# Performance work log

Measured on AMD Instinct MI355X. Metric: run time of the kernel, lower is better.

Reference implementation:

```python
import jax, jax.numpy as jnp
import numpy as np

B, N_NODE, FN, FE = 8, 128, 64, 64  # batch, n_node, n_node_fea, n_edge_fea


def setup_inputs() -> dict:
    key = jax.random.key(0)
    k = jax.random.split(key, 7)
    stdv_w = 1.0 / np.sqrt(2 * FN + FE)  # torch reset uses 1/sqrt(size(0))
    stdv_b = 1.0 / np.sqrt(FN)
    return {
        "H": jax.random.normal(k[0], (B, N_NODE, FN), jnp.float32),
        "A": jax.random.uniform(k[1], (B, N_NODE, N_NODE), jnp.float32),
        "E": jax.random.normal(k[2], (B, N_NODE, N_NODE, FE), jnp.float32),
        "W_att": jax.random.uniform(k[3], (2 * FN + FE, FN), jnp.float32, -stdv_w, stdv_w),
        "W_nei": jax.random.uniform(k[4], (2 * FN + FE, FN), jnp.float32, -stdv_w, stdv_w),
        "bias_att": jax.random.uniform(k[5], (FN,), jnp.float32, -stdv_b, stdv_b),
        "bias_nei": jax.random.uniform(k[6], (FN,), jnp.float32, -stdv_b, stdv_b),
        "N": N_NODE,
    }


def _branch(H, A, E, W, bias, fn):
    # (A[...,None] * cat(H_i, H_j, E)) @ W + bias, computed without
    # materializing the [B,N,N,2F+Fe] concat: split W into row blocks.
    f = H.shape[-1]
    Wi, Wj, We = W[:f], W[f:2 * f], W[2 * f:]
    proj = (
        jnp.einsum('bif,fl->bil', H, Wi)[:, :, None, :]   # H_i broadcast over j
        + jnp.einsum('bjf,fl->bjl', H, Wj)[:, None, :, :] # H_j broadcast over i
        + jnp.einsum('bije,el->bijl', E, We)
    )
    return A[..., None] * proj + bias  # [B, N, N, F]


def reference(H, A, E, W_att, W_nei, bias_att, bias_nei, N):
    att = _branch(H, A, E, W_att, bias_att, None)
    conv = _branch(H, A, E, W_nei, bias_nei, None)
    gated = jax.nn.sigmoid(att) * jax.nn.relu(conv)  # [B, N, N, F]
    return jnp.sum(gated, axis=1)  # sum over first node axis -> [B, N, F]
```

## Files before the change

### kernel.cpp

```cpp
#include <hip/hip_runtime.h>


typedef _Float16 half8 __attribute__((ext_vector_type(8)));
typedef float floatx4 __attribute__((ext_vector_type(4)));

__device__ __forceinline__ half8 cvt2(const float4 a, const float4 b) {
  half8 v;
  v[0] = (_Float16)a.x; v[1] = (_Float16)a.y; v[2] = (_Float16)a.z; v[3] = (_Float16)a.w;
  v[4] = (_Float16)b.x; v[5] = (_Float16)b.y; v[6] = (_Float16)b.z; v[7] = (_Float16)b.w;
  return v;
}

__global__ __launch_bounds__(256, 2)
void amp_fused(const float* __restrict__ H, const float* __restrict__ A,
               const float* __restrict__ E,
               const float* __restrict__ Wa, const float* __restrict__ Wn,
               const float* __restrict__ ba, const float* __restrict__ bn,
               float* __restrict__ out) {
  const int bx = blockIdx.x;
  const int b = bx >> 6;
  const int rem = bx & 63;
  const int jt = rem >> 3;
  const int ch = rem & 7;
  const int w = threadIdx.x >> 6;
  const int lane = threadIdx.x & 63;
  const int quad = lane >> 4;
  const int l15 = lane & 15;
  const int i0b = ch * 16;
  const int i0 = i0b + w * 4;
  const int j0 = jt * 16;
  const float* Wptr[2] = {Wa, Wn};

  __shared__ __align__(16) char smem[48 * 1024];
  _Float16* fraglds = reinterpret_cast<_Float16*>(smem);
  float* pflds = reinterpret_cast<float*>(smem);
  float* pjlds = reinterpret_cast<float*>(smem + 8 * 1024);
  float (*red)[16][64] = reinterpret_cast<float (*)[16][64]>(smem);

  half8 hi[2], hj[2];
  {
    const float* hib = H + (b * 128 + i0b + l15) * 64 + quad * 8;
    const float* hjb = H + (b * 128 + j0 + l15) * 64 + quad * 8;
#pragma unroll
    for (int hh = 0; hh < 2; ++hh) {
      hi[hh] = cvt2(*reinterpret_cast<const float4*>(hib + hh * 32),
                    *reinterpret_cast<const float4*>(hib + hh * 32 + 4));
      hj[hh] = cvt2(*reinterpret_cast<const float4*>(hjb + hh * 32),
                    *reinterpret_cast<const float4*>(hjb + hh * 32 + 4));
    }
  }

#pragma unroll
  for (int k = 0; k < 12; ++k) {
    const int F = w * 12 + k;
    const int kind = F >> 4;
    const int f = F & 15;
    const int br = f >> 3;
    const int t = (f >> 1) & 3;
    const int hh = f & 1;
    const float* src = Wptr[br] + (kind * 64 + hh * 32 + quad * 8) * 64 + t * 16 + l15;
    half8 v;
#pragma unroll
    for (int x = 0; x < 8; ++x) v[x] = (_Float16)src[x * 64];
    *reinterpret_cast<half8*>(fraglds + F * 512 + lane * 8) = v;
  }
  __syncthreads();

  floatx4 pif[2], pjf[2];
#pragma unroll
  for (int pp = 0; pp < 2; ++pp) {
    const int p = w * 2 + pp;
    const int br = p >> 2;
    const int t = p & 3;
    floatx4 z = {0.f, 0.f, 0.f, 0.f};
    pif[pp] = z; pjf[pp] = z;
#pragma unroll
    for (int hh = 0; hh < 2; ++hh) {
      half8 bi = *reinterpret_cast<half8*>(fraglds + (br * 8 + t * 2 + hh) * 512 + lane * 8);
      half8 bj = *reinterpret_cast<half8*>(fraglds + (16 + br * 8 + t * 2 + hh) * 512 + lane * 8);
      pif[pp] = __builtin_amdgcn_mfma_f32_16x16x32_f16(hi[hh], bi, pif[pp], 0, 0, 0);
      pjf[pp] = __builtin_amdgcn_mfma_f32_16x16x32_f16(hj[hh], bj, pjf[pp], 0, 0, 0);
    }
  }
  __syncthreads();
#pragma unroll
  for (int pp = 0; pp < 2; ++pp) {
    const int p = w * 2 + pp;
    *reinterpret_cast<floatx4*>(pflds + (p * 64 + lane) * 4) = pif[pp];
    *reinterpret_cast<floatx4*>(pjlds + (p * 64 + lane) * 4) = pjf[pp];
  }
  __syncthreads();

  float pia_all[2][4][4];
  float pj[2][4][4];
  half8 wf[2][4][2];
#pragma unroll
  for (int br = 0; br < 2; ++br)
#pragma unroll
    for (int t = 0; t < 4; ++t) {
      const int p = br * 4 + t;
      const floatx4 pjv = *reinterpret_cast<const floatx4*>(pjlds + (p * 64 + lane) * 4);
      const floatx4 piv = *reinterpret_cast<const floatx4*>(pflds + (p * 64 + w * 16 + l15) * 4);
#pragma unroll
      for (int r = 0; r < 4; ++r) { pj[br][t][r] = pjv[r]; pia_all[br][t][r] = piv[r]; }
#pragma unroll
      for (int hh = 0; hh < 2; ++hh)
        wf[br][t][hh] = *reinterpret_cast<half8*>(
            fraglds + (32 + br * 8 + t * 2 + hh) * 512 + lane * 8);
    }

  float biasv[2][4];
#pragma unroll
  for (int t = 0; t < 4; ++t) {
    biasv[0][t] = ba[t * 16 + l15];
    biasv[1][t] = bn[t * 16 + l15];
  }

  float acc[4][4];
#pragma unroll
  for (int t = 0; t < 4; ++t)
#pragma unroll
    for (int r = 0; r < 4; ++r) acc[t][r] = 0.f;

#pragma unroll
  for (int ii = 0; ii < 4; ++ii) {
    const int i = i0 + ii;
    const float* erow = E + ((size_t)((b * 128 + i) * 128 + j0 + l15)) * 64 + quad * 8;
    half8 a0 = cvt2(*reinterpret_cast<const float4*>(erow),
                    *reinterpret_cast<const float4*>(erow + 4));
    half8 a1 = cvt2(*reinterpret_cast<const float4*>(erow + 32),
                    *reinterpret_cast<const float4*>(erow + 36));

    const float4 av4 = *reinterpret_cast<const float4*>(
        A + (b * 128 + i) * 128 + j0 + quad * 4);
    const float av[4] = {av4.x, av4.y, av4.z, av4.w};

#pragma unroll
    for (int t = 0; t < 4; ++t) {
      floatx4 z = {0.f, 0.f, 0.f, 0.f};
      floatx4 pa = __builtin_amdgcn_mfma_f32_16x16x32_f16(a0, wf[0][t][0], z, 0, 0, 0);
      pa = __builtin_amdgcn_mfma_f32_16x16x32_f16(a1, wf[0][t][1], pa, 0, 0, 0);
      floatx4 pn = __builtin_amdgcn_mfma_f32_16x16x32_f16(a0, wf[1][t][0], z, 0, 0, 0);
      pn = __builtin_amdgcn_mfma_f32_16x16x32_f16(a1, wf[1][t][1], pn, 0, 0, 0);
#pragma unroll
      for (int r = 0; r < 4; ++r) {
        float att = av[r] * (pa[r] + pia_all[0][t][ii] + pj[0][t][r]) + biasv[0][t];
        float cnv = av[r] * (pn[r] + pia_all[1][t][ii] + pj[1][t][r]) + biasv[1][t];
        float ex = __expf(-att);
        float sig = __builtin_amdgcn_rcpf(1.0f + ex);
        acc[t][r] += sig * fmaxf(cnv, 0.f);
      }
    }
  }

  __syncthreads();
#pragma unroll
  for (int t = 0; t < 4; ++t)
#pragma unroll
    for (int r = 0; r < 4; ++r)
      red[w][quad * 4 + r][t * 16 + l15] = acc[t][r];
  __syncthreads();

  const int tid = threadIdx.x;
#pragma unroll
  for (int k = 0; k < 4; ++k) {
    int idx = k * 256 + tid;
    int jl = idx >> 6;
    int l = idx & 63;
    float s = red[0][jl][l] + red[1][jl][l] + red[2][jl][l] + red[3][jl][l];
    atomicAdd(out + (b * 128 + j0 + jl) * 64 + l, s);
  }
}

extern "C" void kernel_launch(void* const* d_in, const int* in_sizes, int n_in,
                              void* d_out, int out_size, void* d_ws, size_t ws_size,
                              hipStream_t stream) {
  const float* H = (const float*)d_in[0];
  const float* A = (const float*)d_in[1];
  const float* E = (const float*)d_in[2];
  const float* Wa = (const float*)d_in[3];
  const float* Wn = (const float*)d_in[4];
  const float* ba = (const float*)d_in[5];
  const float* bn = (const float*)d_in[6];
  float* out = (float*)d_out;

  hipMemsetAsync(d_out, 0, (size_t)out_size * sizeof(float), stream);
  amp_fused<<<512, 256, 0, stream>>>(H, A, E, Wa, Wn, ba, bn, out);
}
```

Measured before the change: 97.46 us.

## Prefetch first E/A rows before weight staging and trim conversions and barriers

Loads the E and A data for the first two i-rows, plus the bias values, at kernel start, so their global-memory latency overlaps the weight fp16 staging and the H projections. The projection scratch moves to its own LDS region (64KB total), which removes one barrier; another barrier before the reduction writes is also dropped. Float-to-half conversions now use packed round-toward-zero instructions, which slightly changes rounding. The prefetched data raises register pressure under the 2-blocks-per-CU launch bound.

```diff
diff --git a/kernel.cpp b/kernel.cpp
--- a/kernel.cpp
+++ b/kernel.cpp
@@ -2,13 +2,16 @@
 
 
 typedef _Float16 half8 __attribute__((ext_vector_type(8)));
+typedef __fp16 fp16x2 __attribute__((ext_vector_type(2)));
 typedef float floatx4 __attribute__((ext_vector_type(4)));
 
 __device__ __forceinline__ half8 cvt2(const float4 a, const float4 b) {
-  half8 v;
-  v[0] = (_Float16)a.x; v[1] = (_Float16)a.y; v[2] = (_Float16)a.z; v[3] = (_Float16)a.w;
-  v[4] = (_Float16)b.x; v[5] = (_Float16)b.y; v[6] = (_Float16)b.z; v[7] = (_Float16)b.w;
-  return v;
+  union { fp16x2 h2[4]; half8 h8; } u;
+  u.h2[0] = __builtin_amdgcn_cvt_pkrtz(a.x, a.y);
+  u.h2[1] = __builtin_amdgcn_cvt_pkrtz(a.z, a.w);
+  u.h2[2] = __builtin_amdgcn_cvt_pkrtz(b.x, b.y);
+  u.h2[3] = __builtin_amdgcn_cvt_pkrtz(b.z, b.w);
+  return u.h8;
 }
 
 __global__ __launch_bounds__(256, 2)
@@ -31,11 +34,30 @@
   const int j0 = jt * 16;
   const float* Wptr[2] = {Wa, Wn};
 
-  __shared__ __align__(16) char smem[48 * 1024];
+  __shared__ __align__(16) char smem[64 * 1024];
   _Float16* fraglds = reinterpret_cast<_Float16*>(smem);
-  float* pflds = reinterpret_cast<float*>(smem);
-  float* pjlds = reinterpret_cast<float*>(smem + 8 * 1024);
+  float* pflds = reinterpret_cast<float*>(smem + 48 * 1024);
+  float* pjlds = reinterpret_cast<float*>(smem + 56 * 1024);
   float (*red)[16][64] = reinterpret_cast<float (*)[16][64]>(smem);
+
+  float4 e_pf[2][4];
+  float4 a_pf[2];
+#pragma unroll
+  for (int ii = 0; ii < 2; ++ii) {
+    const float* erow = E + ((size_t)((b * 128 + i0 + ii) * 128 + j0 + l15)) * 64 + quad * 8;
+    e_pf[ii][0] = *reinterpret_cast<const float4*>(erow);
+    e_pf[ii][1] = *reinterpret_cast<const float4*>(erow + 4);
+    e_pf[ii][2] = *reinterpret_cast<const float4*>(erow + 32);
+    e_pf[ii][3] = *reinterpret_cast<const float4*>(erow + 36);
+    a_pf[ii] = *reinterpret_cast<const float4*>(A + (b * 128 + i0 + ii) * 128 + j0 + quad * 4);
+  }
+
+  float biasv[2][4];
+#pragma unroll
+  for (int t = 0; t < 4; ++t) {
+    biasv[0][t] = ba[t * 16 + l15];
+    biasv[1][t] = bn[t * 16 + l15];
+  }
 
   half8 hi[2], hj[2];
   {
@@ -59,10 +81,11 @@
     const int t = (f >> 1) & 3;
     const int hh = f & 1;
     const float* src = Wptr[br] + (kind * 64 + hh * 32 + quad * 8) * 64 + t * 16 + l15;
-    half8 v;
-#pragma unroll
-    for (int x = 0; x < 8; ++x) v[x] = (_Float16)src[x * 64];
-    *reinterpret_cast<half8*>(fraglds + F * 512 + lane * 8) = v;
+    union { fp16x2 h2[4]; half8 h8; } u;
+#pragma unroll
+    for (int x = 0; x < 4; ++x)
+      u.h2[x] = __builtin_amdgcn_cvt_pkrtz(src[(2 * x) * 64], src[(2 * x + 1) * 64]);
+    *reinterpret_cast<half8*>(fraglds + F * 512 + lane * 8) = u.h8;
   }
   __syncthreads();
 
@@ -82,7 +105,6 @@
       pjf[pp] = __builtin_amdgcn_mfma_f32_16x16x32_f16(hj[hh], bj, pjf[pp], 0, 0, 0);
     }
   }
-  __syncthreads();
 #pragma unroll
   for (int pp = 0; pp < 2; ++pp) {
     const int p = w * 2 + pp;
@@ -109,13 +131,6 @@
             fraglds + (32 + br * 8 + t * 2 + hh) * 512 + lane * 8);
     }
 
-  float biasv[2][4];
-#pragma unroll
-  for (int t = 0; t < 4; ++t) {
-    biasv[0][t] = ba[t * 16 + l15];
-    biasv[1][t] = bn[t * 16 + l15];
-  }
-
   float acc[4][4];
 #pragma unroll
   for (int t = 0; t < 4; ++t)
@@ -125,15 +140,22 @@
 #pragma unroll
   for (int ii = 0; ii < 4; ++ii) {
     const int i = i0 + ii;
-    const float* erow = E + ((size_t)((b * 128 + i) * 128 + j0 + l15)) * 64 + quad * 8;
-    half8 a0 = cvt2(*reinterpret_cast<const float4*>(erow),
-                    *reinterpret_cast<const float4*>(erow + 4));
-    half8 a1 = cvt2(*reinterpret_cast<const float4*>(erow + 32),
-                    *reinterpret_cast<const float4*>(erow + 36));
-
-    const float4 av4 = *reinterpret_cast<const float4*>(
-        A + (b * 128 + i) * 128 + j0 + quad * 4);
-    const float av[4] = {av4.x, av4.y, av4.z, av4.w};
+    half8 a0, a1;
+    float av[4];
+    if (ii < 2) {
+      a0 = cvt2(e_pf[ii][0], e_pf[ii][1]);
+      a1 = cvt2(e_pf[ii][2], e_pf[ii][3]);
+      av[0] = a_pf[ii].x; av[1] = a_pf[ii].y; av[2] = a_pf[ii].z; av[3] = a_pf[ii].w;
+    } else {
+      const float* erow = E + ((size_t)((b * 128 + i) * 128 + j0 + l15)) * 64 + quad * 8;
+      a0 = cvt2(*reinterpret_cast<const float4*>(erow),
+                *reinterpret_cast<const float4*>(erow + 4));
+      a1 = cvt2(*reinterpret_cast<const float4*>(erow + 32),
+                *reinterpret_cast<const float4*>(erow + 36));
+      const float4 av4 = *reinterpret_cast<const float4*>(
+          A + (b * 128 + i) * 128 + j0 + quad * 4);
+      av[0] = av4.x; av[1] = av4.y; av[2] = av4.z; av[3] = av4.w;
+    }
 
 #pragma unroll
     for (int t = 0; t < 4; ++t) {
@@ -153,7 +175,6 @@
     }
   }
 
-  __syncthreads();
 #pragma unroll
   for (int t = 0; t < 4; ++t)
 #pragma unroll
```

Measured after the change: 95.09 us. 1.02x faster.
